# Kernel optimization log

Measured on AMD Instinct MI355X. Metric: run time of the kernel, lower is better.

## Reference

```python
import jax, jax.numpy as jnp
import numpy as np

B, S, D_IN, D_FC1, NB = 16384, 256, 2048, 1024, 10

def setup_inputs() -> dict:
    key = jax.random.key(0)
    k1, k2, k3, k4 = jax.random.split(key, 4)
    return {
        "input_feats": jax.random.normal(k1, (B, D_IN), dtype=jnp.float32),
        "w1": jax.random.normal(k2, (D_IN, D_FC1), dtype=jnp.float32) * 0.02,
        "b1": jnp.zeros((D_FC1,), dtype=jnp.float32),
        "w_shape": jax.random.normal(k3, (D_FC1, 2 * NB), dtype=jnp.float32) * 0.02,
        "b_shape": jnp.zeros((2 * NB,), dtype=jnp.float32),
        "noise": jax.random.normal(k4, (B, S, NB), dtype=jnp.float32),
        "num_samples": S,
    }

def reference(input_feats, w1, b1, w_shape, b_shape, noise, num_samples):
    # x = ELU(fc1(input_feats))
    x = jax.nn.elu(input_feats @ w1 + b1)                      # (B, 1024)
    shape_params = x @ w_shape + b_shape                       # (B, 20)
    shape_mode = shape_params[:, :NB]                          # (B, 10)
    shape_log_std = shape_params[:, NB:]                       # (B, 10)
    # Normal(mode, exp(log_std)).rsample([num_samples]).transpose(0,1)
    # reparameterized with externalized eps -> (B, num_samples, 10)
    shape_samples = shape_mode[:, None, :] + jnp.exp(shape_log_std)[:, None, :] * noise
    return shape_mode, shape_log_std, shape_samples
```

## Files before the change

kernel.cpp:

```cpp
#include <hip/hip_runtime.h>
#include <stdint.h>

using f32x4  = __attribute__((ext_vector_type(4))) float;
using bf16x8 = __attribute__((ext_vector_type(8))) short;
using ushort8 = __attribute__((ext_vector_type(8))) unsigned short;

#define B_   16384
#define S_   256
#define DIN  2048
#define DFC  1024
#define NB_  10

__device__ __forceinline__ unsigned short f2bf(float f) {
  union { float f; unsigned int u; } v; v.f = f;
  unsigned int u = v.u;
  unsigned int r = (u + 0x7FFFu + ((u >> 16) & 1u)) >> 16;
  return (unsigned short)r;
}

__device__ __forceinline__ void gload_lds16(const void* g, void* l) {
  __builtin_amdgcn_global_load_lds(
      (const __attribute__((address_space(1))) unsigned int*)g,
      (__attribute__((address_space(3))) unsigned int*)l, 16, 0, 0);
}

__device__ __forceinline__ int SW(int r) {
  return ((r & 3) << 3) | (r & 4) | ((r >> 3) * 3);
}

__global__ __launch_bounds__(256)
void convT_kernel(const float* __restrict__ W, unsigned short* __restrict__ Wt) {
  __shared__ unsigned short t[32][33];
  const int tx = threadIdx.x & 31;
  const int ty = threadIdx.x >> 5;
  const int nb = blockIdx.x * 32;
  const int kb = blockIdx.y * 32;
#pragma unroll
  for (int i = 0; i < 32; i += 8)
    t[ty + i][tx] = f2bf(W[(size_t)(kb + ty + i) * DFC + nb + tx]);
  __syncthreads();
#pragma unroll
  for (int i = 0; i < 32; i += 8)
    Wt[(size_t)(nb + ty + i) * DIN + kb + tx] = t[tx][ty + i];
}

__global__ __launch_bounds__(256)
void convW2_kernel(const float* __restrict__ Wsh, unsigned short* __restrict__ WshT) {
  const int idx = blockIdx.x * 256 + threadIdx.x;
  const int j = idx >> 10, k = idx & 1023;
  WshT[idx] = (j < 20) ? f2bf(Wsh[(size_t)k * 20 + j]) : (unsigned short)0;
}

__global__ __launch_bounds__(256)
void convA_kernel(const float* __restrict__ A, unsigned short* __restrict__ Ab) {
  const size_t total = (size_t)B_ * DIN;
  size_t idx = ((size_t)blockIdx.x * 256 + threadIdx.x) * 8;
  const size_t stride = (size_t)gridDim.x * 256 * 8;
  for (; idx < total; idx += stride) {
    f32x4 a = *(const f32x4*)(A + idx);
    f32x4 b = *(const f32x4*)(A + idx + 4);
    ushort8 o;
    o[0] = f2bf(a[0]); o[1] = f2bf(a[1]); o[2] = f2bf(a[2]); o[3] = f2bf(a[3]);
    o[4] = f2bf(b[0]); o[5] = f2bf(b[1]); o[6] = f2bf(b[2]); o[7] = f2bf(b[3]);
    *(ushort8*)(Ab + idx) = o;
  }
}

__global__ __launch_bounds__(512, 2)
void gemm1_kernel(const unsigned short* __restrict__ Ab, const unsigned short* __restrict__ Bt,
                  const unsigned short* __restrict__ WshT, const float* __restrict__ b1,
                  float* __restrict__ part) {
  __shared__ unsigned short sT[2][2][2][8192];
  const int tid  = threadIdx.x;
  const int wave = tid >> 6, lane = tid & 63;
  const int wm = wave >> 2, wn = wave & 3;
  const int b = blockIdx.x;
  const int tile = (b & 7) * 32 + (b >> 3);
  const int mtile = tile >> 2, ntile = tile & 3;
  const int rowBase = mtile * 256, colBase = ntile * 256;

  f32x4 acc[8][4] = {};
  bf16x8 a0[4], a1[4];
  bf16x8 b0[2], b1v[2];
  bf16x8 c0[2], c1[2];

  const int lrow0 = wave * 16 + (lane >> 3);
  const int q     = (lane & 7) ^ (lrow0 & 7);
  const unsigned short* gA = Ab + (size_t)(rowBase + lrow0 * 2 + (q >> 2)) * DIN + (q & 3) * 8;
  const unsigned short* gB = Bt + (size_t)(colBase + lrow0 * 2 + (q >> 2)) * DIN + (q & 3) * 8;
  const int ldOff = wave * 1024;

  const int frow = lane & 15, hi = lane >> 4, fr2 = frow >> 1;
  const int pp    = ((frow & 1) * 4 + hi) ^ fr2;
  const int aBase = (wm * 64 + fr2) * 64 + pp * 8;
  const int bBase = (wn * 32 + fr2) * 64 + pp * 8;

#define STAGE(opv, db, ksv, kt) do {                                        \
    const unsigned short* g_ = ((opv) ? gB : gA) + (kt) * 64 + (ksv) * 32;  \
    unsigned short* l_ = &sT[db][opv][ksv][ldOff];                          \
    gload_lds16(g_, l_);                                                    \
    gload_lds16(g_ + (size_t)16 * DIN, l_ + 512);                           \
  } while (0)
#define RDA4(db, ksv, mq, dst) do {                                         \
    const unsigned short* s_ = &sT[db][0][ksv][aBase + (mq) * 2048];        \
    dst[0] = *(const bf16x8*)(s_);        dst[1] = *(const bf16x8*)(s_ + 512); \
    dst[2] = *(const bf16x8*)(s_ + 1024); dst[3] = *(const bf16x8*)(s_ + 1536); \
  } while (0)
#define RDB2(db, ksv, ni, dst) do {                                         \
    const unsigned short* s_ = &sT[db][1][ksv][bBase + (ni) * 1024];        \
    dst[0] = *(const bf16x8*)(s_);        dst[1] = *(const bf16x8*)(s_ + 512); \
  } while (0)
#define MMQ(MB, NB0, X0, X1) do {                                           \
    __builtin_amdgcn_s_setprio(1);                                          \
    _Pragma("unroll") for (int mm = 0; mm < 4; ++mm)                        \
    _Pragma("unroll") for (int nn = 0; nn < 2; ++nn) {                      \
      acc[(MB)+mm][(NB0)+nn] = __builtin_amdgcn_mfma_f32_16x16x32_bf16(     \
          a0[mm], X0[nn], acc[(MB)+mm][(NB0)+nn], 0, 0, 0);                 \
      acc[(MB)+mm][(NB0)+nn] = __builtin_amdgcn_mfma_f32_16x16x32_bf16(     \
          a1[mm], X1[nn], acc[(MB)+mm][(NB0)+nn], 0, 0, 0);                 \
    }                                                                       \
    __builtin_amdgcn_s_setprio(0);                                          \
  } while (0)
#define FENCE asm volatile("" ::: "memory")
#define BARP do { FENCE; __builtin_amdgcn_s_barrier();                      \
                  __builtin_amdgcn_sched_barrier(0); } while (0)

  STAGE(0, 0, 0, 0); STAGE(1, 0, 0, 0);
  STAGE(0, 0, 1, 0); STAGE(1, 0, 1, 0);
  STAGE(0, 1, 0, 1); STAGE(1, 1, 0, 1);
  asm volatile("s_waitcnt vmcnt(2)" ::: "memory");
  BARP;

  const int NT = DIN / 64;
#pragma unroll 2
  for (int t = 0; t < NT; ++t) {
    const int db = t & 1, dn = db ^ 1;
    RDA4(db, 0, 0, a0); RDA4(db, 1, 0, a1);
    RDB2(db, 0, 0, b0); RDB2(db, 1, 0, b1v);
    if (t < NT - 1) STAGE(0, dn, 1, t + 1);
    BARP;
    MMQ(0, 0, b0, b1v);
    BARP;
    RDB2(db, 0, 1, c0); RDB2(db, 1, 1, c1);
    if (t < NT - 1) STAGE(1, dn, 1, t + 1);
    BARP;
    MMQ(0, 2, c0, c1);
    BARP;
    RDA4(db, 0, 1, a0); RDA4(db, 1, 1, a1);
    BARP;
    MMQ(4, 0, b0, b1v);
    BARP;
    if (t < NT - 2) { STAGE(0, db, 0, t + 2); STAGE(1, db, 0, t + 2); }
    BARP;
    MMQ(4, 2, c0, c1);
    if (t < NT - 2)       asm volatile("s_waitcnt vmcnt(4)" ::: "memory");
    else if (t == NT - 2) asm volatile("s_waitcnt vmcnt(0)" ::: "memory");
    BARP;
  }
#undef STAGE
#undef RDA4
#undef RDB2
#undef MMQ

  const int ec0l = wn * 64 + frow;
  float bv[4];
#pragma unroll
  for (int n = 0; n < 4; ++n) bv[n] = b1[colBase + ec0l + n * 16];

  unsigned short* sX = (unsigned short*)sT;
  BARP;

#pragma unroll
  for (int h = 0; h < 2; ++h) {
#pragma unroll
    for (int mm = 0; mm < 4; ++mm) {
#pragma unroll
      for (int n = 0; n < 4; ++n) {
#pragma unroll
        for (int r = 0; r < 4; ++r) {
          float v = acc[h * 4 + mm][n][r] + bv[n];
          v = v > 0.f ? v : expm1f(v);
          const int lrow = wm * 64 + mm * 16 + hi * 4 + r;
          const int cel  = ec0l + n * 16;
          const int p    = (cel >> 3) ^ SW(lrow & 15);
          sX[lrow * 256 + p * 8 + (cel & 7)] = f2bf(v);
        }
      }
    }
    BARP;
    f32x4 acc2[2] = {};
    const int rb = wave * 16;
#pragma unroll
    for (int ks = 0; ks < 8; ++ks) {
      const int p = (ks * 4 + hi) ^ SW(frow);
      bf16x8 xa = *(const bf16x8*)&sX[(rb + frow) * 256 + p * 8];
      bf16x8 w0 = *(const bf16x8*)(WshT + (size_t)frow * DFC + colBase + ks * 32 + hi * 8);
      bf16x8 w1 = *(const bf16x8*)(WshT + (size_t)(16 + frow) * DFC + colBase + ks * 32 + hi * 8);
      acc2[0] = __builtin_amdgcn_mfma_f32_16x16x32_bf16(xa, w0, acc2[0], 0, 0, 0);
      acc2[1] = __builtin_amdgcn_mfma_f32_16x16x32_bf16(xa, w1, acc2[1], 0, 0, 0);
    }
#pragma unroll
    for (int jf = 0; jf < 2; ++jf) {
      const int j = jf * 16 + frow;
      if (j < 20) {
#pragma unroll
        for (int r = 0; r < 4; ++r) {
          const int lrow = rb + hi * 4 + r;
          const int grow = rowBase + h * 64 + (lrow & 63) + (lrow >> 6) * 128;
          part[(size_t)ntile * (B_ * 20) + (size_t)grow * 20 + j] = acc2[jf][r];
        }
      }
    }
    BARP;
  }
}

__global__ __launch_bounds__(256)
void reduce2_kernel(const float* __restrict__ part, const float* __restrict__ bsh,
                    float* __restrict__ out) {
  const int idx = blockIdx.x * 256 + threadIdx.x;
  if (idx >= B_ * 20) return;
  const int row = idx / 20, j = idx - row * 20;
  float s = bsh[j];
#pragma unroll
  for (int t = 0; t < 4; ++t) s += part[(size_t)t * (B_ * 20) + idx];
  const int jj = j < 10 ? j : j - 10;
  const size_t base = (j < 10) ? (size_t)0 : (size_t)B_ * NB_;
  out[base + (size_t)row * NB_ + jj] = s;
}

__global__ __launch_bounds__(256)
void sample_kernel(const float* __restrict__ noise, float* __restrict__ out) {
  __shared__ float sm[4][NB_], se[4][NB_];
  const int tid  = threadIdx.x;
  const int wave = tid >> 6, lane = tid & 63;
  const int row  = blockIdx.x * 4 + wave;
  if (lane < NB_) {
    sm[wave][lane] = out[(size_t)row * NB_ + lane];
    se[wave][lane] = expf(out[(size_t)B_ * NB_ + (size_t)row * NB_ + lane]);
  }
  __syncthreads();
  const f32x4* np4 = (const f32x4*)(noise + (size_t)row * (S_ * NB_));
  f32x4*       op4 = (f32x4*)(out + (size_t)2 * B_ * NB_ + (size_t)row * (S_ * NB_));
#pragma unroll
  for (int it = 0; it < (S_ * NB_) / 256; ++it) {
    f32x4 nv = np4[it * 64 + lane];
    int j0 = (lane * 4 + it * 6) % 10;
    int j1 = j0 + 1; if (j1 >= 10) j1 -= 10;
    int j2 = j1 + 1; if (j2 >= 10) j2 -= 10;
    int j3 = j2 + 1; if (j3 >= 10) j3 -= 10;
    f32x4 r;
    r[0] = sm[wave][j0] + se[wave][j0] * nv[0];
    r[1] = sm[wave][j1] + se[wave][j1] * nv[1];
    r[2] = sm[wave][j2] + se[wave][j2] * nv[2];
    r[3] = sm[wave][j3] + se[wave][j3] * nv[3];
    op4[it * 64 + lane] = r;
  }
}

extern "C" void kernel_launch(void* const* d_in, const int* in_sizes, int n_in,
                              void* d_out, int out_size, void* d_ws, size_t ws_size,
                              hipStream_t stream) {
  const float* A     = (const float*)d_in[0];
  const float* W1    = (const float*)d_in[1];
  const float* b1    = (const float*)d_in[2];
  const float* Wsh   = (const float*)d_in[3];
  const float* bsh   = (const float*)d_in[4];
  const float* noise = (const float*)d_in[5];
  float* out = (float*)d_out;

  unsigned short* Wt   = (unsigned short*)d_ws;
  unsigned short* WshT = Wt + (size_t)DFC * DIN;
  const size_t wsNeed = (size_t)DFC * DIN * 2 + 65536 +
                        (size_t)4 * B_ * 20 * 4 + (size_t)B_ * DIN * 2;
  float* part;
  unsigned short* Ab;
  if (ws_size >= wsNeed) {
    part = (float*)(WshT + 32 * 1024);
    Ab   = (unsigned short*)(part + (size_t)4 * B_ * 20);
  } else {
    part = out + (size_t)2 * B_ * NB_;
    Ab   = (unsigned short*)(part + (size_t)4 * B_ * 20);
  }

  convT_kernel<<<dim3(DFC / 32, DIN / 32), 256, 0, stream>>>(W1, Wt);
  convW2_kernel<<<dim3(128), 256, 0, stream>>>(Wsh, WshT);
  convA_kernel<<<dim3(2048), 256, 0, stream>>>(A, Ab);
  gemm1_kernel<<<dim3((B_ / 256) * (DFC / 256)), 512, 0, stream>>>(Ab, Wt, WshT, b1, part);
  reduce2_kernel<<<dim3((B_ * 20 + 255) / 256), 256, 0, stream>>>(part, bsh, out);
  sample_kernel<<<dim3(B_ / 4), 256, 0, stream>>>(noise, out);
}
```

Before: 182.8 us.

## Shrink GEMM1 K-tile to 32 with simple double buffering

Replaces the two-stage-ahead, 64-wide K pipeline with 32-wide K tiles, a single double buffer, and one MFMA half per A fragment set. This halves LDS use and cuts the register fragments and barriers per iteration. In exchange, each iteration now fully drains outstanding global loads before the barrier, so there is less prefetch depth to hide memory latency, and the loop runs twice as many iterations.

```diff
diff --git a/kernel.cpp b/kernel.cpp
--- a/kernel.cpp
+++ b/kernel.cpp
@@ -70,7 +70,7 @@
 void gemm1_kernel(const unsigned short* __restrict__ Ab, const unsigned short* __restrict__ Bt,
                   const unsigned short* __restrict__ WshT, const float* __restrict__ b1,
                   float* __restrict__ part) {
-  __shared__ unsigned short sT[2][2][2][8192];
+  __shared__ unsigned short sT[2][2][8192];
   const int tid  = threadIdx.x;
   const int wave = tid >> 6, lane = tid & 63;
   const int wm = wave >> 2, wn = wave & 3;
@@ -80,9 +80,7 @@
   const int rowBase = mtile * 256, colBase = ntile * 256;
 
   f32x4 acc[8][4] = {};
-  bf16x8 a0[4], a1[4];
-  bf16x8 b0[2], b1v[2];
-  bf16x8 c0[2], c1[2];
+  bf16x8 a0[4], a1[4], bfr[4];
 
   const int lrow0 = wave * 16 + (lane >> 3);
   const int q     = (lane & 7) ^ (lrow0 & 7);
@@ -95,72 +93,58 @@
   const int aBase = (wm * 64 + fr2) * 64 + pp * 8;
   const int bBase = (wn * 32 + fr2) * 64 + pp * 8;
 
-#define STAGE(opv, db, ksv, kt) do {                                        \
-    const unsigned short* g_ = ((opv) ? gB : gA) + (kt) * 64 + (ksv) * 32;  \
-    unsigned short* l_ = &sT[db][opv][ksv][ldOff];                          \
+#define STG(opv, db, kt) do {                                               \
+    const unsigned short* g_ = ((opv) ? gB : gA) + (kt) * 32;               \
+    unsigned short* l_ = &sT[db][opv][ldOff];                               \
     gload_lds16(g_, l_);                                                    \
     gload_lds16(g_ + (size_t)16 * DIN, l_ + 512);                           \
   } while (0)
-#define RDA4(db, ksv, mq, dst) do {                                         \
-    const unsigned short* s_ = &sT[db][0][ksv][aBase + (mq) * 2048];        \
+#define RDA4(db, mq, dst) do {                                              \
+    const unsigned short* s_ = &sT[db][0][aBase + (mq) * 2048];             \
     dst[0] = *(const bf16x8*)(s_);        dst[1] = *(const bf16x8*)(s_ + 512); \
     dst[2] = *(const bf16x8*)(s_ + 1024); dst[3] = *(const bf16x8*)(s_ + 1536); \
   } while (0)
-#define RDB2(db, ksv, ni, dst) do {                                         \
-    const unsigned short* s_ = &sT[db][1][ksv][bBase + (ni) * 1024];        \
+#define RDB4(db, dst) do {                                                  \
+    const unsigned short* s_ = &sT[db][1][bBase];                           \
     dst[0] = *(const bf16x8*)(s_);        dst[1] = *(const bf16x8*)(s_ + 512); \
-  } while (0)
-#define MMQ(MB, NB0, X0, X1) do {                                           \
+    dst[2] = *(const bf16x8*)(s_ + 1024); dst[3] = *(const bf16x8*)(s_ + 1536); \
+  } while (0)
+#define MMH(MB, Ar) do {                                                    \
     __builtin_amdgcn_s_setprio(1);                                          \
     _Pragma("unroll") for (int mm = 0; mm < 4; ++mm)                        \
-    _Pragma("unroll") for (int nn = 0; nn < 2; ++nn) {                      \
-      acc[(MB)+mm][(NB0)+nn] = __builtin_amdgcn_mfma_f32_16x16x32_bf16(     \
-          a0[mm], X0[nn], acc[(MB)+mm][(NB0)+nn], 0, 0, 0);                 \
-      acc[(MB)+mm][(NB0)+nn] = __builtin_amdgcn_mfma_f32_16x16x32_bf16(     \
-          a1[mm], X1[nn], acc[(MB)+mm][(NB0)+nn], 0, 0, 0);                 \
-    }                                                                       \
+    _Pragma("unroll") for (int nn = 0; nn < 4; ++nn)                        \
+      acc[(MB)+mm][nn] = __builtin_amdgcn_mfma_f32_16x16x32_bf16(           \
+          Ar[mm], bfr[nn], acc[(MB)+mm][nn], 0, 0, 0);                      \
     __builtin_amdgcn_s_setprio(0);                                          \
   } while (0)
 #define FENCE asm volatile("" ::: "memory")
 #define BARP do { FENCE; __builtin_amdgcn_s_barrier();                      \
                   __builtin_amdgcn_sched_barrier(0); } while (0)
 
-  STAGE(0, 0, 0, 0); STAGE(1, 0, 0, 0);
-  STAGE(0, 0, 1, 0); STAGE(1, 0, 1, 0);
-  STAGE(0, 1, 0, 1); STAGE(1, 1, 0, 1);
-  asm volatile("s_waitcnt vmcnt(2)" ::: "memory");
+  STG(0, 0, 0); STG(1, 0, 0);
+  asm volatile("s_waitcnt vmcnt(0)" ::: "memory");
   BARP;
 
-  const int NT = DIN / 64;
+  const int NT = DIN / 32;
 #pragma unroll 2
   for (int t = 0; t < NT; ++t) {
     const int db = t & 1, dn = db ^ 1;
-    RDA4(db, 0, 0, a0); RDA4(db, 1, 0, a1);
-    RDB2(db, 0, 0, b0); RDB2(db, 1, 0, b1v);
-    if (t < NT - 1) STAGE(0, dn, 1, t + 1);
-    BARP;
-    MMQ(0, 0, b0, b1v);
-    BARP;
-    RDB2(db, 0, 1, c0); RDB2(db, 1, 1, c1);
-    if (t < NT - 1) STAGE(1, dn, 1, t + 1);
-    BARP;
-    MMQ(0, 2, c0, c1);
-    BARP;
-    RDA4(db, 0, 1, a0); RDA4(db, 1, 1, a1);
-    BARP;
-    MMQ(4, 0, b0, b1v);
-    BARP;
-    if (t < NT - 2) { STAGE(0, db, 0, t + 2); STAGE(1, db, 0, t + 2); }
-    BARP;
-    MMQ(4, 2, c0, c1);
-    if (t < NT - 2)       asm volatile("s_waitcnt vmcnt(4)" ::: "memory");
-    else if (t == NT - 2) asm volatile("s_waitcnt vmcnt(0)" ::: "memory");
-    BARP;
-  }
-#undef STAGE
+    RDA4(db, 0, a0); RDB4(db, bfr);
+    if (t < NT - 1) STG(0, dn, t + 1);
+    BARP;
+    MMH(0, a0);
+    BARP;
+    RDA4(db, 1, a1);
+    if (t < NT - 1) STG(1, dn, t + 1);
+    BARP;
+    MMH(4, a1);
+    if (t < NT - 1) asm volatile("s_waitcnt vmcnt(0)" ::: "memory");
+    BARP;
+  }
+#undef STG
 #undef RDA4
-#undef RDB2
-#undef MMQ
+#undef RDB4
+#undef MMH
 
   const int ec0l = wn * 64 + frow;
   float bv[4];
```

After: 186.4 us. No clear change (+2.0%).
